# Performance work log

Measured on AMD Instinct MI355X. Metric: run time of the kernel, lower is better.

## Reference

```python
import jax, jax.numpy as jnp
import numpy as np

BT, NQ, NC, C, H, HID = 192, 64, 1024, 384, 8, 1536
DH = C // H                       # 48
SCALE = DH ** -0.5
MAX_NEG = -float(np.finfo(np.float32).max)


def _ln(x, eps, g=None, b=None):
    m = x.mean(-1, keepdims=True)
    v = ((x - m) ** 2).mean(-1, keepdims=True)
    y = (x - m) / jnp.sqrt(v + eps)
    if g is not None:
        y = y * g + b
    return y


def _gelu_tanh(x):
    # GELU(approximate='tanh')
    return 0.5 * x * (1.0 + jnp.tanh(jnp.sqrt(2.0 / jnp.pi) * (x + 0.044715 * x ** 3)))


def setup_inputs() -> dict:
    key = jax.random.key(0)
    ks = jax.random.split(key, 10)
    s = lambda fan: 1.0 / np.sqrt(fan)
    return {
        "x": jax.random.normal(ks[0], (BT, NQ, C), jnp.float32),
        "context": jax.random.normal(ks[1], (BT, NC, C), jnp.float32),
        "mask": jax.random.randint(ks[2], (BT, NQ), 0, 2) > 0,
        "Wq": jax.random.normal(ks[3], (C, C), jnp.float32) * s(C),
        "bq": jnp.zeros((C,), jnp.float32),
        "Wkv": jax.random.normal(ks[4], (C, 2 * C), jnp.float32) * s(C),
        "bkv": jnp.zeros((2 * C,), jnp.float32),
        "Wo": jax.random.normal(ks[5], (C, C), jnp.float32) * s(C),
        "bo": jnp.zeros((C,), jnp.float32),
        "g_ctx": jnp.ones((C,), jnp.float32),
        "b_ctx": jnp.zeros((C,), jnp.float32),
        "W1": jax.random.normal(ks[6], (C, HID), jnp.float32) * s(C),
        "b1": jnp.zeros((HID,), jnp.float32),
        "W2": jax.random.normal(ks[7], (HID, C), jnp.float32) * s(HID),
        "b2": jnp.zeros((C,), jnp.float32),
    }


def reference(x, context, mask, Wq, bq, Wkv, bkv, Wo, bo, g_ctx, b_ctx, W1, b1, W2, b2):
    # --- cross-attention branch ---
    xn = _ln(x, 1e-6)                       # norm1 (no affine)
    cn = _ln(context, 1e-5, g_ctx, b_ctx)   # norm_context (affine, default eps)
    q = (xn @ Wq + bq).reshape(BT, NQ, H, DH).transpose(0, 2, 1, 3)    # (B,H,NQ,DH)
    kv = cn @ Wkv + bkv
    k, v = jnp.split(kv, 2, axis=-1)
    k = k.reshape(BT, NC, H, DH).transpose(0, 2, 1, 3)                 # (B,H,NC,DH)
    v = v.reshape(BT, NC, H, DH).transpose(0, 2, 1, 3)
    sim = jnp.einsum('bhqd,bhkd->bhqk', q, k) * SCALE                  # (B,H,NQ,NC)
    # mask shape (BT, NQ): True = keep query row; ~mask * (-max) bias
    bias = jnp.where(mask[:, None, :, None], 0.0, MAX_NEG)
    attn = jax.nn.softmax(sim + bias, axis=-1)
    o = jnp.einsum('bhqk,bhkd->bhqd', attn, v).transpose(0, 2, 1, 3).reshape(BT, NQ, C)
    x = x + o @ Wo + bo
    # --- MLP branch ---
    xn2 = _ln(x, 1e-6)                      # norm2 (no affine)
    x = x + _gelu_tanh(xn2 @ W1 + b1) @ W2 + b2
    return x
```

## Files before the change

kernel.cpp:

```cpp
#include <hip/hip_runtime.h>
#include <hip/hip_bf16.h>
#include <math.h>

typedef unsigned int  u32;
typedef unsigned short u16;
typedef unsigned char u8;

#define BTn   192
#define NQn   64
#define NCn   1024
#define Cd    384
#define Hn    8
#define DHn   48
#define HIDn  1536
#define ROWSX (BTn*NQn)
#define ROWSC (BTn*NCn)
#define ATT_SCALE 0.14433756729740643f
#define CBc   64

typedef __bf16 bf16x8 __attribute__((ext_vector_type(8)));
typedef float  f32x4  __attribute__((ext_vector_type(4)));

#define GLL16(gp, lp) __builtin_amdgcn_global_load_lds( \
    (const __attribute__((address_space(1))) void*)(gp), \
    (__attribute__((address_space(3))) void*)(lp), 16, 0, 0)

__device__ __forceinline__ float bf2f(u32 u) {
  union { u32 i; float f; } v; v.i = u << 16; return v.f;
}
__device__ __forceinline__ u16 f2bf(float f) {
  union { float f; u32 i; } v; v.f = f;
  u32 x = v.i;
  x += 0x7fffu + ((x >> 16) & 1u);
  return (u16)(x >> 16);
}
__device__ __forceinline__ void decode8(uint4 r, float* v) {
  v[0]=bf2f(r.x & 0xffffu); v[1]=bf2f(r.x >> 16);
  v[2]=bf2f(r.y & 0xffffu); v[3]=bf2f(r.y >> 16);
  v[4]=bf2f(r.z & 0xffffu); v[5]=bf2f(r.z >> 16);
  v[6]=bf2f(r.w & 0xffffu); v[7]=bf2f(r.w >> 16);
}
__device__ __forceinline__ float gelu_f(float x) {
  float x3 = x*x*x;
  float z = 0.7978845608028654f*x + 0.035677408136300125f*x3;
  float e = __expf(2.f*z);
  float th = 1.f - 2.f/(e+1.f);
  return 0.5f*x*(1.f+th);
}

__global__ void decode_mask_kernel(const u8* __restrict__ m, u8* __restrict__ keep) {
  __shared__ int flags[3];
  int t = threadIdx.x;
  if (t < 3) flags[t] = 0;
  __syncthreads();
  int nonbin = 0, oddset = 0, low01 = 0;
  for (int i = t; i < ROWSX; i += 256) {
    u32 b = m[i];
    if (b > 1u) nonbin = 1;
    if ((i & 3) && b) oddset = 1;
    if (((i & 3) < 2) && b) low01 = 1;
  }
  if (nonbin) flags[0] = 1;
  if (oddset) flags[1] = 1;
  if (low01)  flags[2] = 1;
  __syncthreads();
  int mode = flags[0] ? (flags[2] ? 2 : 3) : (flags[1] ? 1 : 0);
  for (int i = t; i < ROWSX; i += 256) {
    u8 k;
    if (mode == 2)      k = (m[2*i] | m[2*i+1]) ? 1 : 0;
    else if (mode == 3) k = (((const float*)m)[i] != 0.f) ? 1 : 0;
    else if (mode == 1) k = m[i] ? 1 : 0;
    else                k = (((const int*)m)[i] != 0) ? 1 : 0;
    keep[i] = k;
  }
}

template<int AFF, int SRCF32>
__global__ __launch_bounds__(256) void lnorm_kernel(
    const void* __restrict__ srcv, const float* __restrict__ gw,
    const float* __restrict__ bw, u16* __restrict__ dst, float eps)
{
  const int row  = blockIdx.x * 4 + (threadIdx.x >> 6);
  const int lane = threadIdx.x & 63;
  float v[6];
  if (SRCF32) {
    const float2* p = (const float2*)((const float*)srcv + (size_t)row*Cd);
    #pragma unroll
    for (int i = 0; i < 3; i++) { float2 u = p[lane + 64*i]; v[2*i]=u.x; v[2*i+1]=u.y; }
  } else {
    const u32* p = (const u32*)((const u16*)srcv + (size_t)row*Cd);
    #pragma unroll
    for (int i = 0; i < 3; i++) { u32 u = p[lane + 64*i]; v[2*i]=bf2f(u&0xffffu); v[2*i+1]=bf2f(u>>16); }
  }
  float s  = v[0]+v[1]+v[2]+v[3]+v[4]+v[5];
  float s2 = v[0]*v[0]+v[1]*v[1]+v[2]*v[2]+v[3]*v[3]+v[4]*v[4]+v[5]*v[5];
  #pragma unroll
  for (int o = 32; o >= 1; o >>= 1) { s += __shfl_xor(s, o); s2 += __shfl_xor(s2, o); }
  float mean = s * (1.0f/Cd);
  float var  = s2 * (1.0f/Cd) - mean*mean;
  var = var > 0.f ? var : 0.f;
  float rstd = rsqrtf(var + eps);
  u32* d32 = (u32*)(dst + (size_t)row*Cd);
  #pragma unroll
  for (int i = 0; i < 3; i++) {
    float y0 = (v[2*i]   - mean) * rstd;
    float y1 = (v[2*i+1] - mean) * rstd;
    if (AFF) {
      float2 gg = *(const float2*)(gw + 2*(lane + 64*i));
      float2 bb = *(const float2*)(bw + 2*(lane + 64*i));
      y0 = y0*gg.x + bb.x;
      y1 = y1*gg.y + bb.y;
    }
    d32[lane + 64*i] = (u32)f2bf(y0) | ((u32)f2bf(y1) << 16);
  }
}

struct WPack {
  const float* W[5];
  u16* WT[5];
  int K[5];
  int N[5];
  int off[6];
};
__global__ __launch_bounds__(256) void wconvt_all_kernel(WPack p) {
  __shared__ u16 tile[64][66];
  const int bid = blockIdx.x;
  int s = 0;
  #pragma unroll
  for (int i = 1; i < 5; i++) if (bid >= p.off[i]) s = i;
  const float* W = p.W[s];
  u16* WT = p.WT[s];
  const int K = p.K[s], N = p.N[s];
  const int lb = bid - p.off[s];
  const int t  = threadIdx.x;
  const int nt = N >> 6;
  const int bk = lb / nt, bn = lb % nt;
  const int q  = t >> 6;
  const int nl = t & 63;
  #pragma unroll
  for (int r = 0; r < 16; r++) {
    int k = q*16 + r;
    tile[nl][k] = f2bf(W[(size_t)(bk*64 + k)*N + bn*64 + nl]);
  }
  __syncthreads();
  #pragma unroll
  for (int r = 0; r < 16; r++) {
    int n = q*16 + r;
    WT[(size_t)(bn*64 + n)*K + bk*64 + nl] = tile[n][nl];
  }
}

template<int GEL, int RES, int RF32, int OF32>
__global__ __launch_bounds__(256) void mgemm_kernel(
    const u16* __restrict__ A, const u16* __restrict__ WT,
    const float* __restrict__ bias, const void* __restrict__ resv,
    void* __restrict__ Coutv, int M, int N, int K, int nx)
{
  __shared__ u16 As[3][4096];
  __shared__ u16 Bs[3][4096];
  const int t = threadIdx.x;
  const int w = t >> 6, l = t & 63, l15 = l & 15, g = l >> 4;

  const int nwg = gridDim.x;
  const int bid = blockIdx.x;
  const int wg  = (bid & 7) * (nwg >> 3) + (bid >> 3);
  const int n0 = (wg % nx) * 128, m0 = (wg / nx) * 128;
  const int wm = (w & 1) * 64, wn = (w >> 1) * 64;

  const int arow = t >> 2;
  const int swk  = (t >> 3) & 3;
  const int acol = ((t & 3) ^ swk) * 8;
  const u16* Ag = A  + (size_t)(m0 + arow) * K + acol;
  const u16* Wg = WT + (size_t)(n0 + arow) * K + acol;
  const size_t rowskip = (size_t)64 * K;

  const int xk   = (l15 >> 1) & 3;
  const int goff = ((g ^ xk) << 3);

  f32x4 acc[4][4];
  #pragma unroll
  for (int i = 0; i < 4; i++)
    #pragma unroll
    for (int j = 0; j < 4; j++) acc[i][j] = (f32x4){0.f, 0.f, 0.f, 0.f};

  const int nIter = K >> 5;

#define STAGE(nb, kk) do { \
    GLL16(Ag + (kk),           &As[nb][t*8]); \
    GLL16(Ag + (kk) + rowskip, &As[nb][2048 + t*8]); \
    GLL16(Wg + (kk),           &Bs[nb][t*8]); \
    GLL16(Wg + (kk) + rowskip, &Bs[nb][2048 + t*8]); \
  } while (0)

#define BODY(BUF, IT) do { \
    const int it_ = (IT); \
    if (it_ + 2 < nIter) { \
      STAGE((BUF + 2) % 3, (it_ + 2) << 5); \
      asm volatile("s_waitcnt vmcnt(8)" ::: "memory"); \
    } else if (it_ + 1 < nIter) { \
      asm volatile("s_waitcnt vmcnt(4)" ::: "memory"); \
    } else { \
      asm volatile("s_waitcnt vmcnt(0)" ::: "memory"); \
    } \
    __builtin_amdgcn_s_barrier(); \
    __builtin_amdgcn_sched_barrier(0); \
    { \
      bf16x8 af[4], bfv[4]; \
      _Pragma("unroll") \
      for (int i = 0; i < 4; i++) \
        af[i] = *(const bf16x8*)&As[BUF][(wm + i*16 + l15)*32 + goff]; \
      _Pragma("unroll") \
      for (int j = 0; j < 4; j++) \
        bfv[j] = *(const bf16x8*)&Bs[BUF][(wn + j*16 + l15)*32 + goff]; \
      _Pragma("unroll") \
      for (int i = 0; i < 4; i++) \
        _Pragma("unroll") \
        for (int j = 0; j < 4; j++) \
          acc[i][j] = __builtin_amdgcn_mfma_f32_16x16x32_bf16(bfv[j], af[i], acc[i][j], 0, 0, 0); \
    } \
    __builtin_amdgcn_sched_barrier(0); \
    __builtin_amdgcn_s_barrier(); \
  } while (0)

  STAGE(0, 0);
  STAGE(1, 32);
  for (int it0 = 0; it0 < nIter; it0 += 3) {
    BODY(0, it0);
    BODY(1, it0 + 1);
    BODY(2, it0 + 2);
  }
#undef BODY
#undef STAGE

  const float* resf = (const float*)resv;
  const u16*   resb = (const u16*)resv;
  float* Cf = (float*)Coutv;
  u16*   Cb = (u16*)Coutv;
  #pragma unroll
  for (int j = 0; j < 4; j++) {
    const int nb = n0 + wn + j*16 + g*4;
    const float4 bv = *(const float4*)&bias[nb];
    #pragma unroll
    for (int i = 0; i < 4; i++) {
      const int m = m0 + wm + i*16 + l15;
      float c0 = acc[i][j][0] + bv.x;
      float c1 = acc[i][j][1] + bv.y;
      float c2 = acc[i][j][2] + bv.z;
      float c3 = acc[i][j][3] + bv.w;
      if (GEL) { c0 = gelu_f(c0); c1 = gelu_f(c1); c2 = gelu_f(c2); c3 = gelu_f(c3); }
      if (RES) {
        if (RF32) {
          float4 r = *(const float4*)&resf[(size_t)m*N + nb];
          c0 += r.x; c1 += r.y; c2 += r.z; c3 += r.w;
        } else {
          uint2 r = *(const uint2*)&resb[(size_t)m*N + nb];
          c0 += bf2f(r.x & 0xffffu); c1 += bf2f(r.x >> 16);
          c2 += bf2f(r.y & 0xffffu); c3 += bf2f(r.y >> 16);
        }
      }
      if (OF32) {
        *(float4*)&Cf[(size_t)m*N + nb] = make_float4(c0, c1, c2, c3);
      } else {
        uint2 pk = make_uint2((u32)f2bf(c0) | ((u32)f2bf(c1) << 16),
                              (u32)f2bf(c2) | ((u32)f2bf(c3) << 16));
        *(uint2*)&Cb[(size_t)m*N + nb] = pk;
      }
    }
  }
}

template<int GEL, int RES, int RF32, int OF32>
__global__ __launch_bounds__(512, 4) void mgemm256_kernel(
    const u16* __restrict__ A, const u16* __restrict__ WT,
    const float* __restrict__ bias, const void* __restrict__ resv,
    void* __restrict__ Coutv, int M, int N, int K, int nx)
{
  __shared__ u16 As[3][4096];
  __shared__ u16 Bs[3][8192];
  const int t = threadIdx.x;
  const int w = t >> 6, l = t & 63, l15 = l & 15, g = l >> 4;

  const int nwg = gridDim.x;
  const int bid = blockIdx.x;
  const int wg  = (bid & 7) * (nwg >> 3) + (bid >> 3);
  const int n0 = (wg % nx) * 256, m0 = (wg / nx) * 128;
  const int wm = (w & 1) * 64, wn = (w >> 1) * 64;

  const int arow = t >> 2;
  const int swk  = (t >> 3) & 3;
  const int acol = ((t & 3) ^ swk) * 8;
  const u16* Ag = A  + (size_t)(m0 + arow) * K + acol;
  const u16* Wg = WT + (size_t)(n0 + arow) * K + acol;
  const size_t rowskipB = (size_t)128 * K;

  const int xk   = (l15 >> 1) & 3;
  const int goff = ((g ^ xk) << 3);

  f32x4 acc[4][4];
  #pragma unroll
  for (int i = 0; i < 4; i++)
    #pragma unroll
    for (int j = 0; j < 4; j++) acc[i][j] = (f32x4){0.f, 0.f, 0.f, 0.f};

  const int nIter = K >> 5;

#define STAGE(nb, kk) do { \
    GLL16(Ag + (kk),            &As[nb][t*8]); \
    GLL16(Wg + (kk),            &Bs[nb][t*8]); \
    GLL16(Wg + (kk) + rowskipB, &Bs[nb][4096 + t*8]); \
  } while (0)

#define BODY(BUF, IT) do { \
    const int it_ = (IT); \
    if (it_ + 2 < nIter) { \
      STAGE((BUF + 2) % 3, (it_ + 2) << 5); \
      asm volatile("s_waitcnt vmcnt(6)" ::: "memory"); \
    } else if (it_ + 1 < nIter) { \
      asm volatile("s_waitcnt vmcnt(3)" ::: "memory"); \
    } else { \
      asm volatile("s_waitcnt vmcnt(0)" ::: "memory"); \
    } \
    __builtin_amdgcn_s_barrier(); \
    __builtin_amdgcn_sched_barrier(0); \
    { \
      bf16x8 af[4], bfv[4]; \
      _Pragma("unroll") \
      for (int i = 0; i < 4; i++) \
        af[i] = *(const bf16x8*)&As[BUF][(wm + i*16 + l15)*32 + goff]; \
      _Pragma("unroll") \
      for (int j = 0; j < 4; j++) \
        bfv[j] = *(const bf16x8*)&Bs[BUF][(wn + j*16 + l15)*32 + goff]; \
      _Pragma("unroll") \
      for (int i = 0; i < 4; i++) \
        _Pragma("unroll") \
        for (int j = 0; j < 4; j++) \
          acc[i][j] = __builtin_amdgcn_mfma_f32_16x16x32_bf16(bfv[j], af[i], acc[i][j], 0, 0, 0); \
    } \
    __builtin_amdgcn_sched_barrier(0); \
    __builtin_amdgcn_s_barrier(); \
  } while (0)

  STAGE(0, 0);
  STAGE(1, 32);
  for (int it0 = 0; it0 < nIter; it0 += 3) {
    BODY(0, it0);
    BODY(1, it0 + 1);
    BODY(2, it0 + 2);
  }
#undef BODY
#undef STAGE

  const float* resf = (const float*)resv;
  const u16*   resb = (const u16*)resv;
  float* Cf = (float*)Coutv;
  u16*   Cb = (u16*)Coutv;
  #pragma unroll
  for (int j = 0; j < 4; j++) {
    const int nb = n0 + wn + j*16 + g*4;
    const float4 bv = *(const float4*)&bias[nb];
    #pragma unroll
    for (int i = 0; i < 4; i++) {
      const int m = m0 + wm + i*16 + l15;
      float c0 = acc[i][j][0] + bv.x;
      float c1 = acc[i][j][1] + bv.y;
      float c2 = acc[i][j][2] + bv.z;
      float c3 = acc[i][j][3] + bv.w;
      if (GEL) { c0 = gelu_f(c0); c1 = gelu_f(c1); c2 = gelu_f(c2); c3 = gelu_f(c3); }
      if (RES) {
        if (RF32) {
          float4 r = *(const float4*)&resf[(size_t)m*N + nb];
          c0 += r.x; c1 += r.y; c2 += r.z; c3 += r.w;
        } else {
          uint2 r = *(const uint2*)&resb[(size_t)m*N + nb];
          c0 += bf2f(r.x & 0xffffu); c1 += bf2f(r.x >> 16);
          c2 += bf2f(r.y & 0xffffu); c3 += bf2f(r.y >> 16);
        }
      }
      if (OF32) {
        *(float4*)&Cf[(size_t)m*N + nb] = make_float4(c0, c1, c2, c3);
      } else {
        uint2 pk = make_uint2((u32)f2bf(c0) | ((u32)f2bf(c1) << 16),
                              (u32)f2bf(c2) | ((u32)f2bf(c3) << 16));
        *(uint2*)&Cb[(size_t)m*N + nb] = pk;
      }
    }
  }
}

__global__ __launch_bounds__(256) void fattn_kernel(
    const u16* __restrict__ qb, const u16* __restrict__ kvb,
    const u8* __restrict__ keep, u16* __restrict__ ob, int b0)
{
  __shared__ u16 Qs[64*72];
  __shared__ u16 Ks[64*72];
  __shared__ u16 Vt[48*72];
  __shared__ u16 Ps[4][16*72];

  const int t = threadIdx.x;
  const int w = t >> 6, l = t & 63, l15 = l & 15, g = l >> 4;
  const int h = blockIdx.x, bz = blockIdx.y;
  const int b = b0 + bz;
  const int wq = w * 16;
  const int krow0 = t / 6, kp0 = t % 6;
  const int krow1 = (256 + t) / 6, kp1 = (256 + t) % 6;
  const int vdq = (t >> 4) * 4, vkq = (t & 15) * 4;

  for (int i = t; i < 2304; i += 256) { ((u32*)Qs)[i] = 0; ((u32*)Ks)[i] = 0; }
  __syncthreads();

  for (int i = t; i < 384; i += 256) {
    int row = i / 6, p = i % 6;
    uint4 v4 = *(const uint4*)(qb + (size_t)(b*NQn + row)*Cd + h*DHn + p*8);
    float f[8]; decode8(v4, f);
    u16 e[8];
    #pragma unroll
    for (int j = 0; j < 8; j++) e[j] = f2bf(f[j] * ATT_SCALE);
    uint4 pk = make_uint4((u32)e[0] | ((u32)e[1] << 16), (u32)e[2] | ((u32)e[3] << 16),
                          (u32)e[4] | ((u32)e[5] << 16), (u32)e[6] | ((u32)e[7] << 16));
    *(uint4*)&Qs[row*72 + p*8] = pk;
  }

  u32 kw = *(const u32*)&keep[b*NQn + wq + g*4];
  float kf[4];
  #pragma unroll
  for (int r = 0; r < 4; r++) kf[r] = ((kw >> (8*r)) & 0xffu) ? 1.f : 0.f;

  float mrow[4], lrow[4];
  f32x4 oacc[3];
  #pragma unroll
  for (int r = 0; r < 4; r++) { mrow[r] = -3.0e38f; lrow[r] = 0.f; }
  #pragma unroll
  for (int d = 0; d < 3; d++) oacc[d] = (f32x4){0.f, 0.f, 0.f, 0.f};

  auto loadKV = [&](int kt, uint4& KR0, uint4& KR1, uint2* V) {
    const u16* base = kvb + ((size_t)bz*NCn + (size_t)kt*64) * (2*(size_t)Cd);
    KR0 = *(const uint4*)(base + (size_t)krow0*(2*Cd) + h*DHn + kp0*8);
    if (t < 128)
      KR1 = *(const uint4*)(base + (size_t)krow1*(2*Cd) + h*DHn + kp1*8);
    if (t < 192) {
      const u16* vs = base + (size_t)vkq*(2*Cd) + Cd + h*DHn + vdq;
      V[0] = *(const uint2*)(vs);
      V[1] = *(const uint2*)(vs + 2*Cd);
      V[2] = *(const uint2*)(vs + 4*Cd);
      V[3] = *(const uint2*)(vs + 6*Cd);
    }
  };
  auto writeKV = [&](const uint4& KR0, const uint4& KR1, const uint2* V) {
    *(uint4*)&Ks[krow0*72 + kp0*8] = KR0;
    if (t < 128) *(uint4*)&Ks[krow1*72 + kp1*8] = KR1;
    if (t < 192) {
      #pragma unroll
      for (int jj = 0; jj < 4; jj++) {
        u16 o4[4] = {((const u16*)&V[0])[jj], ((const u16*)&V[1])[jj],
                     ((const u16*)&V[2])[jj], ((const u16*)&V[3])[jj]};
        *(uint2*)&Vt[(vdq+jj)*72 + vkq] = *(uint2*)o4;
      }
    }
  };

  bf16x8 qf0, qf1;
  auto compute = [&]() {
    f32x4 sf[4];
    #pragma unroll
    for (int f = 0; f < 4; f++) {
      bf16x8 ka = *(const bf16x8*)&Ks[(f*16 + l15)*72 + g*8];
      bf16x8 kb = *(const bf16x8*)&Ks[(f*16 + l15)*72 + 32 + g*8];
      f32x4 z = (f32x4){0.f, 0.f, 0.f, 0.f};
      z = __builtin_amdgcn_mfma_f32_16x16x32_bf16(qf0, ka, z, 0, 0, 0);
      sf[f] = __builtin_amdgcn_mfma_f32_16x16x32_bf16(qf1, kb, z, 0, 0, 0);
    }
    float p[4][4], sc_[4];
    #pragma unroll
    for (int r = 0; r < 4; r++) {
      float pmax = fmaxf(fmaxf(sf[0][r], sf[1][r]), fmaxf(sf[2][r], sf[3][r]));
      #pragma unroll
      for (int s = 1; s < 16; s <<= 1) pmax = fmaxf(pmax, __shfl_xor(pmax, s));
      float mn = kf[r] > 0.f ? fmaxf(mrow[r], pmax) : 0.f;
      sc_[r] = kf[r] > 0.f ? __expf(mrow[r] - mn) : 1.f;
      mrow[r] = mn;
      float p0 = kf[r] > 0.f ? __expf(sf[0][r] - mn) : 1.f;
      float p1 = kf[r] > 0.f ? __expf(sf[1][r] - mn) : 1.f;
      float p2 = kf[r] > 0.f ? __expf(sf[2][r] - mn) : 1.f;
      float p3 = kf[r] > 0.f ? __expf(sf[3][r] - mn) : 1.f;
      p[0][r]=p0; p[1][r]=p1; p[2][r]=p2; p[3][r]=p3;
      float ps = p0+p1+p2+p3;
      #pragma unroll
      for (int s = 1; s < 16; s <<= 1) ps += __shfl_xor(ps, s);
      lrow[r] = lrow[r]*sc_[r] + ps;
      oacc[0][r] *= sc_[r]; oacc[1][r] *= sc_[r]; oacc[2][r] *= sc_[r];
    }
    #pragma unroll
    for (int f = 0; f < 4; f++)
      #pragma unroll
      for (int r = 0; r < 4; r++)
        Ps[w][(g*4 + r)*72 + f*16 + l15] = f2bf(p[f][r]);
    bf16x8 pa0 = *(const bf16x8*)&Ps[w][l15*72 + g*8];
    bf16x8 pa1 = *(const bf16x8*)&Ps[w][l15*72 + 32 + g*8];
    #pragma unroll
    for (int df = 0; df < 3; df++) {
      bf16x8 vb0 = *(const bf16x8*)&Vt[(df*16 + l15)*72 + g*8];
      bf16x8 vb1 = *(const bf16x8*)&Vt[(df*16 + l15)*72 + 32 + g*8];
      oacc[df] = __builtin_amdgcn_mfma_f32_16x16x32_bf16(pa0, vb0, oacc[df], 0, 0, 0);
      oacc[df] = __builtin_amdgcn_mfma_f32_16x16x32_bf16(pa1, vb1, oacc[df], 0, 0, 0);
    }
  };

  uint4 ka0, ka1, kb0_, kb1_;
  uint2 va[4], vb_[4];
  loadKV(0, ka0, ka1, va);
  __syncthreads();

  qf0 = *(const bf16x8*)&Qs[(wq + l15)*72 + g*8];
  qf1 = *(const bf16x8*)&Qs[(wq + l15)*72 + 32 + g*8];

  for (int kt = 0; kt < 16; kt += 2) {
    writeKV(ka0, ka1, va);
    asm volatile("s_waitcnt lgkmcnt(0)" ::: "memory");
    __builtin_amdgcn_sched_barrier(0);
    __builtin_amdgcn_s_barrier();
    __builtin_amdgcn_sched_barrier(0);
    loadKV(kt + 1, kb0_, kb1_, vb_);
    compute();
    __builtin_amdgcn_sched_barrier(0);
    __builtin_amdgcn_s_barrier();
    writeKV(kb0_, kb1_, vb_);
    asm volatile("s_waitcnt lgkmcnt(0)" ::: "memory");
    __builtin_amdgcn_sched_barrier(0);
    __builtin_amdgcn_s_barrier();
    __builtin_amdgcn_sched_barrier(0);
    if (kt + 2 < 16) loadKV(kt + 2, ka0, ka1, va);
    compute();
    if (kt + 2 < 16) {
      __builtin_amdgcn_sched_barrier(0);
      __builtin_amdgcn_s_barrier();
    }
  }

  #pragma unroll
  for (int r = 0; r < 4; r++) {
    float inv = 1.f / lrow[r];
    size_t qrow = (size_t)(b*NQn + wq + g*4 + r);
    #pragma unroll
    for (int df = 0; df < 3; df++)
      ob[qrow*Cd + h*DHn + df*16 + l15] = f2bf(oacc[df][r] * inv);
  }
}

extern "C" void kernel_launch(void* const* d_in, const int* in_sizes, int n_in,
                              void* d_out, int out_size, void* d_ws, size_t ws_size,
                              hipStream_t stream) {
  (void)in_sizes; (void)n_in; (void)out_size; (void)ws_size;
  const float* x   = (const float*)d_in[0];
  const float* ctx = (const float*)d_in[1];
  const u8*    msk = (const u8*)   d_in[2];
  const float* Wq  = (const float*)d_in[3];
  const float* bq  = (const float*)d_in[4];
  const float* Wkv = (const float*)d_in[5];
  const float* bkv = (const float*)d_in[6];
  const float* Wo  = (const float*)d_in[7];
  const float* bo  = (const float*)d_in[8];
  const float* gc  = (const float*)d_in[9];
  const float* bc  = (const float*)d_in[10];
  const float* W1  = (const float*)d_in[11];
  const float* b1  = (const float*)d_in[12];
  const float* W2  = (const float*)d_in[13];
  const float* b2  = (const float*)d_in[14];
  float* out = (float*)d_out;

  char* ws = (char*)d_ws;
  size_t off = 0;
  auto bump = [&](size_t bytes) -> size_t {
    size_t o = off; off += (bytes + 255) & ~(size_t)255; return o;
  };
  const size_t act = (size_t)ROWSX * Cd * 2;
  size_t o_keep = bump(ROWSX);
  size_t o_xn   = bump(act);
  size_t o_x1n  = bump(act);
  size_t o_q    = bump(act);
  size_t o_ob   = bump(act);
  size_t o_x1   = bump(act);
  size_t o_hid  = bump((size_t)ROWSX * HIDn * 2);
  size_t o_wtq  = bump((size_t)Cd*Cd*2);
  size_t o_wtkv = bump((size_t)Cd*2*Cd*2);
  size_t o_wto  = bump((size_t)Cd*Cd*2);
  size_t o_wt1  = bump((size_t)Cd*HIDn*2);
  size_t o_wt2  = bump((size_t)HIDn*Cd*2);
  size_t o_cn   = bump((size_t)CBc * NCn * Cd * 2);
  size_t o_kv   = bump((size_t)CBc * NCn * 2 * Cd * 2);

  u8*  keep = (u8*)(ws + o_keep);
  u16* xn   = (u16*)(ws + o_xn);
  u16* x1n  = (u16*)(ws + o_x1n);
  u16* qb   = (u16*)(ws + o_q);
  u16* obuf = (u16*)(ws + o_ob);
  u16* x1b  = (u16*)(ws + o_x1);
  u16* hidb = (u16*)(ws + o_hid);
  u16* wtq  = (u16*)(ws + o_wtq);
  u16* wtkv = (u16*)(ws + o_wtkv);
  u16* wto  = (u16*)(ws + o_wto);
  u16* wt1  = (u16*)(ws + o_wt1);
  u16* wt2  = (u16*)(ws + o_wt2);
  u16* cnb  = (u16*)(ws + o_cn);
  u16* kvb  = (u16*)(ws + o_kv);

  decode_mask_kernel<<<1, 256, 0, stream>>>(msk, keep);

  WPack wp;
  wp.W[0]=Wq;  wp.WT[0]=wtq;  wp.K[0]=Cd;   wp.N[0]=Cd;
  wp.W[1]=Wkv; wp.WT[1]=wtkv; wp.K[1]=Cd;   wp.N[1]=2*Cd;
  wp.W[2]=Wo;  wp.WT[2]=wto;  wp.K[2]=Cd;   wp.N[2]=Cd;
  wp.W[3]=W1;  wp.WT[3]=wt1;  wp.K[3]=Cd;   wp.N[3]=HIDn;
  wp.W[4]=W2;  wp.WT[4]=wt2;  wp.K[4]=HIDn; wp.N[4]=Cd;
  wp.off[0]=0; wp.off[1]=36; wp.off[2]=108; wp.off[3]=144; wp.off[4]=288; wp.off[5]=432;
  wconvt_all_kernel<<<432, 256, 0, stream>>>(wp);

  lnorm_kernel<0,1><<<ROWSX/4, 256, 0, stream>>>(x, nullptr, nullptr, xn, 1e-6f);

  mgemm_kernel<0,0,0,0><<<3*(ROWSX/128), 256, 0, stream>>>(
      xn, wtq, bq, nullptr, qb, ROWSX, Cd, Cd, 3);

  for (int b0 = 0; b0 < BTn; b0 += CBc) {
    lnorm_kernel<1,1><<<CBc*NCn/4, 256, 0, stream>>>(
        ctx + (size_t)b0*NCn*Cd, gc, bc, cnb, 1e-5f);
    mgemm256_kernel<0,0,0,0><<<3*(CBc*NCn/128), 512, 0, stream>>>(
        cnb, wtkv, bkv, nullptr, kvb, CBc*NCn, 2*Cd, Cd, 3);
    fattn_kernel<<<dim3(Hn, CBc), 256, 0, stream>>>(qb, kvb, keep, obuf, b0);
  }

  mgemm_kernel<0,1,1,0><<<3*(ROWSX/128), 256, 0, stream>>>(
      obuf, wto, bo, x, x1b, ROWSX, Cd, Cd, 3);

  lnorm_kernel<0,0><<<ROWSX/4, 256, 0, stream>>>(x1b, nullptr, nullptr, x1n, 1e-6f);

  mgemm256_kernel<1,0,0,0><<<6*(ROWSX/128), 512, 0, stream>>>(
      x1n, wt1, b1, nullptr, hidb, ROWSX, HIDn, Cd, 6);

  mgemm_kernel<0,1,0,1><<<3*(ROWSX/128), 256, 0, stream>>>(
      hidb, wt2, b2, x1b, out, ROWSX, Cd, HIDn, 3);
}
```

Baseline: 574.2 us.

## Process full context in single launches and add lazy softmax rescaling

Drops the three-chunk loop over batches, so the context layernorm, the KV GEMM and attention each run as one launch over all 192 batches, using full-size workspace buffers. Inside attention, the online-softmax rescale of the running max, sum and output accumulators now runs only when some row's new max exceeds the stored max by more than 8. Otherwise the stale max is kept, which removes exps and multiplies per tile. This costs extra workspace memory and less L2 reuse between KV write and read, and accepts an exp range of up to e^8 before rescaling.

```diff
diff --git a/kernel.cpp b/kernel.cpp
--- a/kernel.cpp
+++ b/kernel.cpp
@@ -16,7 +16,6 @@
 #define ROWSX (BTn*NQn)
 #define ROWSC (BTn*NCn)
 #define ATT_SCALE 0.14433756729740643f
-#define CBc   64
 
 typedef __bf16 bf16x8 __attribute__((ext_vector_type(8)));
 typedef float  f32x4  __attribute__((ext_vector_type(4)));
@@ -389,7 +388,7 @@
 
 __global__ __launch_bounds__(256) void fattn_kernel(
     const u16* __restrict__ qb, const u16* __restrict__ kvb,
-    const u8* __restrict__ keep, u16* __restrict__ ob, int b0)
+    const u8* __restrict__ keep, u16* __restrict__ ob)
 {
   __shared__ u16 Qs[64*72];
   __shared__ u16 Ks[64*72];
@@ -398,8 +397,7 @@
 
   const int t = threadIdx.x;
   const int w = t >> 6, l = t & 63, l15 = l & 15, g = l >> 4;
-  const int h = blockIdx.x, bz = blockIdx.y;
-  const int b = b0 + bz;
+  const int h = blockIdx.x, b = blockIdx.y;
   const int wq = w * 16;
   const int krow0 = t / 6, kp0 = t % 6;
   const int krow1 = (256 + t) / 6, kp1 = (256 + t) % 6;
@@ -428,12 +426,12 @@
   float mrow[4], lrow[4];
   f32x4 oacc[3];
   #pragma unroll
-  for (int r = 0; r < 4; r++) { mrow[r] = -3.0e38f; lrow[r] = 0.f; }
+  for (int r = 0; r < 4; r++) { mrow[r] = kf[r] > 0.f ? -3.0e38f : 0.f; lrow[r] = 0.f; }
   #pragma unroll
   for (int d = 0; d < 3; d++) oacc[d] = (f32x4){0.f, 0.f, 0.f, 0.f};
 
   auto loadKV = [&](int kt, uint4& KR0, uint4& KR1, uint2* V) {
-    const u16* base = kvb + ((size_t)bz*NCn + (size_t)kt*64) * (2*(size_t)Cd);
+    const u16* base = kvb + ((size_t)b*NCn + (size_t)kt*64) * (2*(size_t)Cd);
     KR0 = *(const uint4*)(base + (size_t)krow0*(2*Cd) + h*DHn + kp0*8);
     if (t < 128)
       KR1 = *(const uint4*)(base + (size_t)krow1*(2*Cd) + h*DHn + kp1*8);
@@ -469,25 +467,37 @@
       z = __builtin_amdgcn_mfma_f32_16x16x32_bf16(qf0, ka, z, 0, 0, 0);
       sf[f] = __builtin_amdgcn_mfma_f32_16x16x32_bf16(qf1, kb, z, 0, 0, 0);
     }
-    float p[4][4], sc_[4];
+    float p[4][4], pmax[4];
     #pragma unroll
     for (int r = 0; r < 4; r++) {
-      float pmax = fmaxf(fmaxf(sf[0][r], sf[1][r]), fmaxf(sf[2][r], sf[3][r]));
+      float pm = fmaxf(fmaxf(sf[0][r], sf[1][r]), fmaxf(sf[2][r], sf[3][r]));
       #pragma unroll
-      for (int s = 1; s < 16; s <<= 1) pmax = fmaxf(pmax, __shfl_xor(pmax, s));
-      float mn = kf[r] > 0.f ? fmaxf(mrow[r], pmax) : 0.f;
-      sc_[r] = kf[r] > 0.f ? __expf(mrow[r] - mn) : 1.f;
-      mrow[r] = mn;
-      float p0 = kf[r] > 0.f ? __expf(sf[0][r] - mn) : 1.f;
-      float p1 = kf[r] > 0.f ? __expf(sf[1][r] - mn) : 1.f;
-      float p2 = kf[r] > 0.f ? __expf(sf[2][r] - mn) : 1.f;
-      float p3 = kf[r] > 0.f ? __expf(sf[3][r] - mn) : 1.f;
+      for (int s = 1; s < 16; s <<= 1) pm = fmaxf(pm, __shfl_xor(pm, s));
+      pmax[r] = pm;
+    }
+    float dm = fmaxf(fmaxf(kf[0]*(pmax[0]-mrow[0]), kf[1]*(pmax[1]-mrow[1])),
+                     fmaxf(kf[2]*(pmax[2]-mrow[2]), kf[3]*(pmax[3]-mrow[3])));
+    if (!__all(dm <= 8.f)) {
+      #pragma unroll
+      for (int r = 0; r < 4; r++) {
+        float mn = kf[r] > 0.f ? fmaxf(mrow[r], pmax[r]) : 0.f;
+        float sc = kf[r] > 0.f ? __expf(mrow[r] - mn) : 1.f;
+        mrow[r] = mn;
+        lrow[r] *= sc;
+        oacc[0][r] *= sc; oacc[1][r] *= sc; oacc[2][r] *= sc;
+      }
+    }
+    #pragma unroll
+    for (int r = 0; r < 4; r++) {
+      float p0 = kf[r] > 0.f ? __expf(sf[0][r] - mrow[r]) : 1.f;
+      float p1 = kf[r] > 0.f ? __expf(sf[1][r] - mrow[r]) : 1.f;
+      float p2 = kf[r] > 0.f ? __expf(sf[2][r] - mrow[r]) : 1.f;
+      float p3 = kf[r] > 0.f ? __expf(sf[3][r] - mrow[r]) : 1.f;
       p[0][r]=p0; p[1][r]=p1; p[2][r]=p2; p[3][r]=p3;
       float ps = p0+p1+p2+p3;
       #pragma unroll
       for (int s = 1; s < 16; s <<= 1) ps += __shfl_xor(ps, s);
-      lrow[r] = lrow[r]*sc_[r] + ps;
-      oacc[0][r] *= sc_[r]; oacc[1][r] *= sc_[r]; oacc[2][r] *= sc_[r];
+      lrow[r] += ps;
     }
     #pragma unroll
     for (int f = 0; f < 4; f++)
@@ -585,8 +595,8 @@
   size_t o_wto  = bump((size_t)Cd*Cd*2);
   size_t o_wt1  = bump((size_t)Cd*HIDn*2);
   size_t o_wt2  = bump((size_t)HIDn*Cd*2);
-  size_t o_cn   = bump((size_t)CBc * NCn * Cd * 2);
-  size_t o_kv   = bump((size_t)CBc * NCn * 2 * Cd * 2);
+  size_t o_cn   = bump((size_t)ROWSC * Cd * 2);
+  size_t o_kv   = bump((size_t)ROWSC * 2 * Cd * 2);
 
   u8*  keep = (u8*)(ws + o_keep);
   u16* xn   = (u16*)(ws + o_xn);
@@ -619,13 +629,10 @@
   mgemm_kernel<0,0,0,0><<<3*(ROWSX/128), 256, 0, stream>>>(
       xn, wtq, bq, nullptr, qb, ROWSX, Cd, Cd, 3);
 
-  for (int b0 = 0; b0 < BTn; b0 += CBc) {
-    lnorm_kernel<1,1><<<CBc*NCn/4, 256, 0, stream>>>(
-        ctx + (size_t)b0*NCn*Cd, gc, bc, cnb, 1e-5f);
-    mgemm256_kernel<0,0,0,0><<<3*(CBc*NCn/128), 512, 0, stream>>>(
-        cnb, wtkv, bkv, nullptr, kvb, CBc*NCn, 2*Cd, Cd, 3);
-    fattn_kernel<<<dim3(Hn, CBc), 256, 0, stream>>>(qb, kvb, keep, obuf, b0);
-  }
+  lnorm_kernel<1,1><<<ROWSC/4, 256, 0, stream>>>(ctx, gc, bc, cnb, 1e-5f);
+  mgemm256_kernel<0,0,0,0><<<3*(ROWSC/128), 512, 0, stream>>>(
+      cnb, wtkv, bkv, nullptr, kvb, ROWSC, 2*Cd, Cd, 3);
+  fattn_kernel<<<dim3(Hn, BTn), 256, 0, stream>>>(qb, kvb, keep, obuf);
 
   mgemm_kernel<0,1,1,0><<<3*(ROWSX/128), 256, 0, stream>>>(
       obuf, wto, bo, x, x1b, ROWSX, Cd, Cd, 3);
```

New measurement: 589.1 us. 1.03x slower.
